# Optimization experiments

Measured on AMD Instinct MI355X. Metric: run time of the kernel, lower is better.

## Reference

```python
import jax, jax.numpy as jnp
import numpy as np

B, N, H, W, C_OUT = 4, 480000, 1024, 1024, 64
PR = (0.0, -39.68, -3.0, 69.12, 39.68, 1.0)  # point cloud range [x0,y0,z0,x1,y1,z1]
BN_EPS = 1e-5


def setup_inputs():
    key = jax.random.key(0)
    ks = iter(jax.random.split(key, 48))
    bidx = jax.random.randint(next(ks), (N,), 0, B).astype(jnp.float32)
    px = jax.random.uniform(next(ks), (N,), minval=PR[0], maxval=PR[3])
    py = jax.random.uniform(next(ks), (N,), minval=PR[1], maxval=PR[4])
    pz = jax.random.uniform(next(ks), (N,), minval=PR[2], maxval=PR[5])
    pi = jax.random.uniform(next(ks), (N,))
    points = jnp.stack([bidx, px, py, pz, pi], axis=1)  # [N,5]

    def w(shape):
        return jax.random.normal(next(ks), shape, jnp.float32) * 0.1

    def bnp(c):
        return (1.0 + 0.1 * jax.random.normal(next(ks), (c,), jnp.float32),
                0.1 * jax.random.normal(next(ks), (c,), jnp.float32),
                0.1 * jax.random.normal(next(ks), (c,), jnp.float32),
                jax.random.uniform(next(ks), (c,), minval=0.5, maxval=1.5))

    g0, be0, m0, v0 = bnp(8)
    g1, be1, m1, v1 = bnp(16)
    g2, be2, m2, v2 = bnp(32)
    g3, be3, m3, v3 = bnp(C_OUT)
    return {
        'points': points, 'batch_size': B,
        'w0': w((8, 2, 3, 3)), 'b0': w((8,)),
        'g0': g0, 'be0': be0, 'm0': m0, 'v0': v0,
        'w1': w((16, 1, 3, 3)), 'b1': w((16,)),  # groups=8 conv: 16 out, 8 in groups
        'g1': g1, 'be1': be1, 'm1': m1, 'v1': v1,
        'wdw': w((16, 1, 3, 3)), 'bdw': w((16,)),
        'wpw': w((32, 16, 1, 1)), 'bpw': w((32,)),
        'g2': g2, 'be2': be2, 'm2': m2, 'v2': v2,
        'w3': w((C_OUT, 32, 3, 3)), 'b3': w((C_OUT,)),
        'g3': g3, 'be3': be3, 'm3': m3, 'v3': v3,
    }


def conv2d(x, wt, b, groups=1, pad=1):
    out = jax.lax.conv_general_dilated(
        x, wt, (1, 1), [(pad, pad), (pad, pad)],
        feature_group_count=groups,
        dimension_numbers=('NCHW', 'OIHW', 'NCHW'))
    return out + b[None, :, None, None]


def bn(x, g, be, m, v):
    s = g * jax.lax.rsqrt(v + BN_EPS)
    return x * s[None, :, None, None] + (be - m * s)[None, :, None, None]


def maxpool2(x):
    return jax.lax.reduce_window(x, -jnp.inf, jax.lax.max,
                                 (1, 1, 2, 2), (1, 1, 2, 2), 'VALID')


def channel_shuffle(x, groups):
    b, c, h, w = x.shape
    return x.reshape(b, groups, c // groups, h, w).transpose(0, 2, 1, 3, 4).reshape(b, c, h, w)


def rasterize(points, batch_size):
    # points: [N,5] = (batch_idx, x, y, z, intensity)
    x_scale = W / (PR[3] - PR[0])
    y_scale = H / (PR[4] - PR[1])
    # PR[0]==0 -> no x shift (matches the source's branch)
    xp = (points[:, 1] * x_scale).astype(jnp.int32)  # trunc toward zero like torch .to(int)
    yp = ((points[:, 2] + (PR[4] - PR[1]) / 2) * y_scale).astype(jnp.int32)
    valid = (xp >= 0) & (xp < W) & (yp >= 0) & (yp < H)
    bi = jnp.where(valid, points[:, 0].astype(jnp.int32), batch_size)  # invalid -> OOB, dropped
    xi = jnp.where(valid, xp, W)
    yi = jnp.where(valid, yp, H)
    bev_z = jnp.full((batch_size, H, W), -10.0, jnp.float32)
    bev_z = bev_z.at[bi, yi, xi].max(points[:, 3], mode='drop')
    bev_i = jnp.zeros((batch_size, H, W), jnp.float32)
    bev_i = bev_i.at[bi, yi, xi].max(points[:, 4], mode='drop')
    return jnp.stack([bev_z, bev_i], axis=1)  # [B,2,H,W]


def reference(points, batch_size, w0, b0, g0, be0, m0, v0, w1, b1, g1, be1, m1, v1,
              wdw, bdw, wpw, bpw, g2, be2, m2, v2, w3, b3, g3, be3, m3, v3):
    x = rasterize(points, batch_size)
    x = jax.nn.relu(bn(conv2d(x, w0, b0), g0, be0, m0, v0))          # x_conv1
    x = maxpool2(x)
    x = jax.nn.relu(bn(conv2d(x, w1, b1, groups=8), g1, be1, m1, v1))  # x_conv2
    x = maxpool2(x)
    x = conv2d(x, wdw, bdw, groups=16)      # depthwise
    x = channel_shuffle(x, 16)              # identity when groups==channels, kept for faithfulness
    x = conv2d(x, wpw, bpw, pad=0)          # pointwise 16->32
    x = jax.nn.relu(bn(x, g2, be2, m2, v2))
    x = jax.nn.relu(bn(conv2d(x, w3, b3), g3, be3, m3, v3))          # x_conv3
    x = maxpool2(x)                         # x_conv4 == spatial_features
    return x
```

## Files before the change

### kernel.cpp

```cpp
#include <hip/hip_runtime.h>
#include <cstddef>

#define H_IN 1024
#define W_IN 1024
#define BN_EPS 1e-5f

typedef float f32x4 __attribute__((ext_vector_type(4)));
typedef _Float16 f16x8 __attribute__((ext_vector_type(8)));

__device__ __forceinline__ unsigned encF(float f) {
    unsigned u = __float_as_uint(f);
    return (u & 0x80000000u) ? ~u : (u | 0x80000000u);
}
__device__ __forceinline__ float decF(unsigned e, float untouched) {
    if (e == 0u) return untouched;
    unsigned bits = (e & 0x80000000u) ? (e ^ 0x80000000u) : ~e;
    return __uint_as_float(bits);
}

__global__ void k_rasterize(const float* __restrict__ pts, unsigned* __restrict__ bev, int n) {
    int i = blockIdx.x * blockDim.x + threadIdx.x;
    if (i >= n) return;
    float fb  = pts[(size_t)i*5+0];
    float px  = pts[(size_t)i*5+1];
    float py  = pts[(size_t)i*5+2];
    float pz  = pts[(size_t)i*5+3];
    float pit = pts[(size_t)i*5+4];
    const float XS = (float)(1024.0/69.12);
    const float YS = (float)(1024.0/79.36);
    int xp = (int)(px * XS);
    int yp = (int)((py + 39.68f) * YS);
    if (xp < 0 || xp >= W_IN || yp < 0 || yp >= H_IN) return;
    int b = (int)fb;
    size_t off = (((size_t)b * H_IN + yp) * W_IN + xp) * 2;
    atomicMax(bev + off,     encF(pz));
    atomicMax(bev + off + 1, encF(pit));
}

__global__ __launch_bounds__(256, 4) void k_conv1(
                        const unsigned* __restrict__ bev, const float* __restrict__ w0,
                        const float* __restrict__ b0, const float* __restrict__ g0,
                        const float* __restrict__ be0, const float* __restrict__ m0,
                        const float* __restrict__ v0, _Float16* __restrict__ out) {
    __shared__ float wS[144];
    __shared__ float sS[8], tS[8];
    int t = threadIdx.x;
    if (t < 144) wS[t] = w0[t];
    if (t < 8) {
        float s = g0[t] / sqrtf(v0[t] + BN_EPS);
        sS[t] = s;
        tS[t] = (b0[t] - m0[t]) * s + be0[t];
    }
    __syncthreads();
    int idx = blockIdx.x * 256 + t;
    int x = idx & 511, y = (idx >> 9) & 511, b = idx >> 18;
    const unsigned* base = bev + (size_t)b * H_IN * W_IN * 2;
    float in[2][4][4];
    #pragma unroll
    for (int r = 0; r < 4; r++) {
        int iy = 2*y - 1 + r;
        #pragma unroll
        for (int cc = 0; cc < 4; cc++) {
            int ix = 2*x - 1 + cc;
            if (iy >= 0 && iy < H_IN && ix >= 0 && ix < W_IN) {
                const unsigned* p2 = base + ((size_t)iy*W_IN + ix)*2;
                in[0][r][cc] = decF(p2[0], -10.0f);
                in[1][r][cc] = decF(p2[1], 0.0f);
            } else {
                in[0][r][cc] = 0.0f;
                in[1][r][cc] = 0.0f;
            }
        }
    }
    f16x8 ov;
    #pragma unroll
    for (int oc = 0; oc < 8; oc++) {
        float mx = 0.0f;
        #pragma unroll
        for (int py = 0; py < 2; py++)
            #pragma unroll
            for (int px = 0; px < 2; px++) {
                float acc = 0.0f;
                #pragma unroll
                for (int c = 0; c < 2; c++)
                    #pragma unroll
                    for (int kh = 0; kh < 3; kh++)
                        #pragma unroll
                        for (int kw = 0; kw < 3; kw++)
                            acc += in[c][py+kh][px+kw] * wS[((oc*2+c)*3+kh)*3+kw];
                acc = fmaxf(acc * sS[oc] + tS[oc], 0.0f);
                mx = fmaxf(mx, acc);
            }
        ov[oc] = (_Float16)mx;
    }
    *(f16x8*)(out + ((size_t)((b*512 + y)*512 + x)) * 8) = ov;
}

__global__ __launch_bounds__(256, 4) void k_conv2(
                        const _Float16* __restrict__ x1, const float* __restrict__ w1,
                        const float* __restrict__ b1, const float* __restrict__ g1,
                        const float* __restrict__ be1, const float* __restrict__ m1,
                        const float* __restrict__ v1, float* __restrict__ out) {
    __shared__ float wS[144];
    __shared__ float sS[16], tS[16];
    int t = threadIdx.x;
    if (t < 144) wS[t] = w1[t];
    if (t < 16) {
        float s = g1[t] / sqrtf(v1[t] + BN_EPS);
        sS[t] = s;
        tS[t] = (b1[t] - m1[t]) * s + be1[t];
    }
    __syncthreads();
    int idx = blockIdx.x * 256 + t;
    int x = idx & 255, y = (idx >> 8) & 255, b = idx >> 16;
    const _Float16* base = x1 + (size_t)b * 512 * 512 * 8;

    f16x8 p[4][4];
    #pragma unroll
    for (int r = 0; r < 4; r++) {
        int iy = 2*y - 1 + r;
        #pragma unroll
        for (int c = 0; c < 4; c++) {
            int ix = 2*x - 1 + c;
            if (iy >= 0 && iy < 512 && ix >= 0 && ix < 512) {
                p[r][c] = *(const f16x8*)(base + ((size_t)iy*512 + ix)*8);
            } else {
                f16x8 z = {0,0,0,0,0,0,0,0};
                p[r][c] = z;
            }
        }
    }

    float* ob = out + (size_t)b * 16 * 256 * 256 + (size_t)y*256 + x;
    #pragma unroll
    for (int g = 0; g < 8; g++) {
        #pragma unroll
        for (int sub = 0; sub < 2; sub++) {
            int oc = g*2 + sub;
            float mx = 0.0f;
            #pragma unroll
            for (int qy = 0; qy < 2; qy++)
                #pragma unroll
                for (int qx = 0; qx < 2; qx++) {
                    float acc = 0.0f;
                    #pragma unroll
                    for (int kh = 0; kh < 3; kh++)
                        #pragma unroll
                        for (int kw = 0; kw < 3; kw++)
                            acc += (float)p[qy+kh][qx+kw][g] * wS[(oc*3+kh)*3+kw];
                    acc = fmaxf(acc * sS[oc] + tS[oc], 0.0f);
                    mx = fmaxf(mx, acc);
                }
            ob[(size_t)oc*65536] = mx;
        }
    }
}

__global__ __launch_bounds__(256, 4) void k_dwpw(
                       const float* __restrict__ x2, const float* __restrict__ wdw,
                       const float* __restrict__ bdw, const float* __restrict__ wpw,
                       const float* __restrict__ bpw, const float* __restrict__ g2,
                       const float* __restrict__ be2, const float* __restrict__ m2,
                       const float* __restrict__ v2, _Float16* __restrict__ out) {
    __shared__ float patch[16*10*36];
    __shared__ float wdwS[144];
    __shared__ float bdwS[16];
    __shared__ float wpwS[512];
    __shared__ float sS[32], tS[32];
    int t = threadIdx.x;
    if (t < 144) wdwS[t] = wdw[t];
    if (t < 16) bdwS[t] = bdw[t];
    for (int i = t; i < 512; i += 256) wpwS[i] = wpw[i];
    if (t < 32) {
        float s = g2[t] / sqrtf(v2[t] + BN_EPS);
        sS[t] = s;
        tS[t] = (bpw[t] - m2[t]) * s + be2[t];
    }

    int bi = blockIdx.x;
    int tx = bi & 7, ty = (bi >> 3) & 31, b = bi >> 8;
    int x0 = tx * 32, y0 = ty * 8;
    const float* base = x2 + (size_t)b * 16 * 256 * 256;

    for (int i = t; i < 16*10*34; i += 256) {
        int ic = i / 340;
        int rem = i - ic * 340;
        int r = rem / 34, c = rem - r * 34;
        int gy = y0 - 1 + r, gx = x0 - 1 + c;
        patch[(ic*10 + r)*36 + c] =
            (gy >= 0 && gy < 256 && gx >= 0 && gx < 256)
                ? base[(size_t)ic*65536 + (size_t)gy*256 + gx] : 0.0f;
    }
    __syncthreads();

    int px = t & 31, pyy = t >> 5;
    int x = x0 + px, y = y0 + pyy;

    float dv[16];
    #pragma unroll
    for (int ic = 0; ic < 16; ic++) {
        float d = bdwS[ic];
        #pragma unroll
        for (int r = 0; r < 3; r++)
            #pragma unroll
            for (int c = 0; c < 3; c++)
                d += patch[(ic*10 + pyy + r)*36 + px + c] * wdwS[ic*9 + r*3 + c];
        dv[ic] = d;
    }

    _Float16* ob = out + ((size_t)((b*256 + y)*256 + x)) * 32;
    #pragma unroll
    for (int q = 0; q < 4; q++) {
        f16x8 ov;
        #pragma unroll
        for (int j = 0; j < 8; j++) {
            int oc = q*8 + j;
            float a = 0.0f;
            #pragma unroll
            for (int ic = 0; ic < 16; ic++)
                a += dv[ic] * wpwS[oc*16+ic];
            ov[j] = (_Float16)fmaxf(a*sS[oc] + tS[oc], 0.0f);
        }
        *(f16x8*)(ob + q*8) = ov;
    }
}

__global__ void k_wprep(const float* __restrict__ w3, const float* __restrict__ b3,
                        const float* __restrict__ g3, const float* __restrict__ be3,
                        const float* __restrict__ m3, const float* __restrict__ v3,
                        _Float16* __restrict__ wh, float* __restrict__ tv) {
    __shared__ float sSh[64];
    int t = threadIdx.x;
    if (t < 64) {
        float s = g3[t] / sqrtf(v3[t] + BN_EPS);
        sSh[t] = s;
        if (blockIdx.x == 0) tv[t] = (b3[t] - m3[t]) * s + be3[t];
    }
    __syncthreads();
    int khw = blockIdx.x;
    for (int i = t; i < 2048; i += 256) {
        int oc = i >> 5;
        wh[khw*2048 + i] = (_Float16)(w3[(size_t)i*9 + khw] * sSh[oc]);
    }
}

__global__ __launch_bounds__(256, 2) void k_conv3m(const _Float16* __restrict__ xh,
                                                   const _Float16* __restrict__ wh,
                                                   const float* __restrict__ tv,
                                                   float* __restrict__ out) {
    __shared__ _Float16 As[10*66*40];
    int t = threadIdx.x;
    int lane = t & 63, w = t >> 6;
    int l15 = lane & 15, l4 = lane >> 4;
    int bi = blockIdx.x;
    int xt = bi & 3, yg = (bi >> 2) & 31, b = bi >> 7;
    int x0 = xt * 64;
    int y0 = yg * 8;

    f16x8 Bf[9][4];
    #pragma unroll
    for (int khw = 0; khw < 9; khw++)
        #pragma unroll
        for (int g = 0; g < 4; g++)
            Bf[khw][g] = *(const f16x8*)(wh + ((khw*64 + g*16 + l15)*32 + 8*l4));

    float tvv[4];
    #pragma unroll
    for (int g = 0; g < 4; g++) tvv[g] = tv[g*16 + l15];

    for (int s = t; s < 660; s += 256) {
        int row = s / 66, px = s - row*66;
        int gy = y0 - 1 + row, gx = x0 - 1 + px;
        float4* dst = (float4*)&As[(row*66 + px)*40];
        if (gy >= 0 && gy < 256 && gx >= 0 && gx < 256) {
            const float4* src = (const float4*)(xh + ((size_t)((b*256 + gy)*256 + gx)) * 32);
            #pragma unroll
            for (int j = 0; j < 4; j++) dst[j] = src[j];
        } else {
            float4 z = make_float4(0.f, 0.f, 0.f, 0.f);
            #pragma unroll
            for (int j = 0; j < 4; j++) dst[j] = z;
        }
    }
    __syncthreads();

    for (int ti = 0; ti < 4; ti++) {
        int ypool = yg*4 + ti;
        f32x4 acc[2][4];
        #pragma unroll
        for (int f = 0; f < 2; f++)
            #pragma unroll
            for (int g = 0; g < 4; g++)
                acc[f][g] = (f32x4){0.f, 0.f, 0.f, 0.f};

        #pragma unroll
        for (int kh = 0; kh < 3; kh++)
            #pragma unroll
            for (int kw = 0; kw < 3; kw++) {
                f16x8 Af[2];
                #pragma unroll
                for (int f = 0; f < 2; f++) {
                    int row = 2*ti + f + kh;
                    int px = w*16 + l15 + kw;
                    Af[f] = *(const f16x8*)&As[(row*66 + px)*40 + 8*l4];
                }
                #pragma unroll
                for (int f = 0; f < 2; f++)
                    #pragma unroll
                    for (int g = 0; g < 4; g++)
                        acc[f][g] = __builtin_amdgcn_mfma_f32_16x16x32_f16(
                            Af[f], Bf[kh*3+kw][g], acc[f][g], 0, 0, 0);
            }

        #pragma unroll
        for (int g = 0; g < 4; g++) {
            int oc = g*16 + l15;
            #pragma unroll
            for (int q = 0; q < 2; q++) {
                float v0 = fmaxf(fmaxf(acc[0][g][2*q]   + tvv[g], 0.f),
                                 fmaxf(acc[0][g][2*q+1] + tvv[g], 0.f));
                float v1 = fmaxf(fmaxf(acc[1][g][2*q]   + tvv[g], 0.f),
                                 fmaxf(acc[1][g][2*q+1] + tvv[g], 0.f));
                int px = x0/2 + w*8 + 2*l4 + q;
                out[(((size_t)b*64 + oc)*128 + ypool)*128 + px] = fmaxf(v0, v1);
            }
        }
    }
}

extern "C" void kernel_launch(void* const* d_in, const int* in_sizes, int n_in,
                              void* d_out, int out_size, void* d_ws, size_t ws_size,
                              hipStream_t stream) {
    const float* points = (const float*)d_in[0];
    int n = in_sizes[0] / 5;
    const float* w0  = (const float*)d_in[2];
    const float* b0  = (const float*)d_in[3];
    const float* g0  = (const float*)d_in[4];
    const float* be0 = (const float*)d_in[5];
    const float* m0  = (const float*)d_in[6];
    const float* v0  = (const float*)d_in[7];
    const float* w1  = (const float*)d_in[8];
    const float* b1  = (const float*)d_in[9];
    const float* g1  = (const float*)d_in[10];
    const float* be1 = (const float*)d_in[11];
    const float* m1  = (const float*)d_in[12];
    const float* v1  = (const float*)d_in[13];
    const float* wdw = (const float*)d_in[14];
    const float* bdw = (const float*)d_in[15];
    const float* wpw = (const float*)d_in[16];
    const float* bpw = (const float*)d_in[17];
    const float* g2  = (const float*)d_in[18];
    const float* be2 = (const float*)d_in[19];
    const float* m2  = (const float*)d_in[20];
    const float* v2  = (const float*)d_in[21];
    const float* w3  = (const float*)d_in[22];
    const float* b3  = (const float*)d_in[23];
    const float* g3  = (const float*)d_in[24];
    const float* be3 = (const float*)d_in[25];
    const float* m3  = (const float*)d_in[26];
    const float* v3  = (const float*)d_in[27];

    float* ws  = (float*)d_ws;
    unsigned* bev = (unsigned*)ws;
    _Float16* x1h = (_Float16*)(ws + 8388608);
    float* x2  = ws;
    _Float16* x3h = (_Float16*)(ws + 8388608);
    _Float16* wh  = (_Float16*)(ws + 16777216);
    float* tv  = ws + 16786432;
    float* outp = (float*)d_out;

    k_wprep<<<9, 256, 0, stream>>>(w3, b3, g3, be3, m3, v3, wh, tv);
    hipMemsetAsync(bev, 0, (size_t)4 * H_IN * W_IN * 2 * sizeof(unsigned), stream);
    k_rasterize<<<(n + 255)/256, 256, 0, stream>>>(points, bev, n);
    k_conv1<<<4096, 256, 0, stream>>>(bev, w0, b0, g0, be0, m0, v0, x1h);
    k_conv2<<<1024, 256, 0, stream>>>(x1h, w1, b1, g1, be1, m1, v1, x2);
    k_dwpw<<<1024, 256, 0, stream>>>(x2, wdw, bdw, wpw, bpw, g2, be2, m2, v2, x3h);
    k_conv3m<<<512, 256, 0, stream>>>(x3h, wh, tv, outp);
}
```

Measured before the change: 142.2 us.

## Rewrite grouped conv2 as MFMA over LDS tile, fuse memset with weight prep

The grouped 3x3 conv2 with maxpool now loads a 10x66 input tile into shared memory and computes it with 16x16x32 f16 MFMA instructions, using per-kw zero-padded weight fragments, instead of per-thread scalar FMAs over a 4x4 register patch. The BEV memset and the conv3 weight prep are merged into one launch, and rasterization uses a grid-stride loop with a quarter as many blocks. The aim is less ALU work in conv2 and fewer launches, at the cost of wasted MFMA lanes and new index mapping that could be wrong.

```diff
diff --git a/kernel.cpp b/kernel.cpp
--- a/kernel.cpp
+++ b/kernel.cpp
@@ -18,23 +18,54 @@
     return __uint_as_float(bits);
 }
 
+__global__ void k_prep(uint4* __restrict__ bevq,
+                       const float* __restrict__ w3, const float* __restrict__ b3,
+                       const float* __restrict__ g3, const float* __restrict__ be3,
+                       const float* __restrict__ m3, const float* __restrict__ v3,
+                       _Float16* __restrict__ wh, float* __restrict__ tv) {
+    int bid = blockIdx.x;
+    int t = threadIdx.x;
+    if (bid < 2048) {
+        int i = bid * 256 + t;
+        uint4 z = {0u, 0u, 0u, 0u};
+        #pragma unroll
+        for (int j = 0; j < 4; j++)
+            bevq[(size_t)j*524288 + i] = z;
+        return;
+    }
+    __shared__ float sSh[64];
+    if (t < 64) {
+        float s = g3[t] / sqrtf(v3[t] + BN_EPS);
+        sSh[t] = s;
+        if (bid == 2048) tv[t] = (b3[t] - m3[t]) * s + be3[t];
+    }
+    __syncthreads();
+    int khw = bid - 2048;
+    for (int i = t; i < 2048; i += 256) {
+        int oc = i >> 5;
+        wh[khw*2048 + i] = (_Float16)(w3[(size_t)i*9 + khw] * sSh[oc]);
+    }
+}
+
 __global__ void k_rasterize(const float* __restrict__ pts, unsigned* __restrict__ bev, int n) {
-    int i = blockIdx.x * blockDim.x + threadIdx.x;
-    if (i >= n) return;
-    float fb  = pts[(size_t)i*5+0];
-    float px  = pts[(size_t)i*5+1];
-    float py  = pts[(size_t)i*5+2];
-    float pz  = pts[(size_t)i*5+3];
-    float pit = pts[(size_t)i*5+4];
+    int i0 = blockIdx.x * blockDim.x + threadIdx.x;
+    int stride = gridDim.x * blockDim.x;
     const float XS = (float)(1024.0/69.12);
     const float YS = (float)(1024.0/79.36);
-    int xp = (int)(px * XS);
-    int yp = (int)((py + 39.68f) * YS);
-    if (xp < 0 || xp >= W_IN || yp < 0 || yp >= H_IN) return;
-    int b = (int)fb;
-    size_t off = (((size_t)b * H_IN + yp) * W_IN + xp) * 2;
-    atomicMax(bev + off,     encF(pz));
-    atomicMax(bev + off + 1, encF(pit));
+    for (int i = i0; i < n; i += stride) {
+        float fb  = pts[(size_t)i*5+0];
+        float px  = pts[(size_t)i*5+1];
+        float py  = pts[(size_t)i*5+2];
+        float pz  = pts[(size_t)i*5+3];
+        float pit = pts[(size_t)i*5+4];
+        int xp = (int)(px * XS);
+        int yp = (int)((py + 39.68f) * YS);
+        if (xp < 0 || xp >= W_IN || yp < 0 || yp >= H_IN) continue;
+        int b = (int)fb;
+        size_t off = (((size_t)b * H_IN + yp) * W_IN + xp) * 2;
+        atomicMax(bev + off,     encF(pz));
+        atomicMax(bev + off + 1, encF(pit));
+    }
 }
 
 __global__ __launch_bounds__(256, 4) void k_conv1(
@@ -96,13 +127,13 @@
     *(f16x8*)(out + ((size_t)((b*512 + y)*512 + x)) * 8) = ov;
 }
 
-__global__ __launch_bounds__(256, 4) void k_conv2(
+__global__ __launch_bounds__(256, 4) void k_conv2m(
                         const _Float16* __restrict__ x1, const float* __restrict__ w1,
                         const float* __restrict__ b1, const float* __restrict__ g1,
                         const float* __restrict__ be1, const float* __restrict__ m1,
                         const float* __restrict__ v1, float* __restrict__ out) {
-    __shared__ float wS[144];
-    __shared__ float sS[16], tS[16];
+    __shared__ _Float16 As[10][66][8];
+    __shared__ float wS[144], sS[16], tS[16];
     int t = threadIdx.x;
     if (t < 144) wS[t] = w1[t];
     if (t < 16) {
@@ -110,48 +141,57 @@
         sS[t] = s;
         tS[t] = (b1[t] - m1[t]) * s + be1[t];
     }
-    __syncthreads();
-    int idx = blockIdx.x * 256 + t;
-    int x = idx & 255, y = (idx >> 8) & 255, b = idx >> 16;
+    int lane = t & 63, w = t >> 6;
+    int l15 = lane & 15, l4 = lane >> 4;
+    int bi = blockIdx.x;
+    int xt = bi & 7, yg = (bi >> 3) & 63, b = bi >> 9;
+    int x0 = xt * 64;
+    int y0 = yg * 8;
+    __syncthreads();
+
+    f16x8 Bf[3];
+    #pragma unroll
+    for (int kh = 0; kh < 3; kh++) {
+        f16x8 z = {0,0,0,0,0,0,0,0};
+        if (l4 < 3) z[l15 >> 1] = (_Float16)(wS[l15*9 + kh*3 + l4] * sS[l15]);
+        Bf[kh] = z;
+    }
+    float tvv = tS[l15];
+
     const _Float16* base = x1 + (size_t)b * 512 * 512 * 8;
-
-    f16x8 p[4][4];
-    #pragma unroll
-    for (int r = 0; r < 4; r++) {
-        int iy = 2*y - 1 + r;
-        #pragma unroll
-        for (int c = 0; c < 4; c++) {
-            int ix = 2*x - 1 + c;
-            if (iy >= 0 && iy < 512 && ix >= 0 && ix < 512) {
-                p[r][c] = *(const f16x8*)(base + ((size_t)iy*512 + ix)*8);
-            } else {
-                f16x8 z = {0,0,0,0,0,0,0,0};
-                p[r][c] = z;
+    for (int s = t; s < 660; s += 256) {
+        int row = s / 66, px = s - row * 66;
+        int gy = y0 - 1 + row, gx = x0 - 1 + px;
+        f16x8 v = {0,0,0,0,0,0,0,0};
+        if (gy >= 0 && gy < 512 && gx >= 0 && gx < 512)
+            v = *(const f16x8*)(base + ((size_t)gy*512 + gx)*8);
+        *(f16x8*)&As[row][px][0] = v;
+    }
+    __syncthreads();
+
+    for (int ti = 0; ti < 4; ti++) {
+        f32x4 acc[2];
+        acc[0] = (f32x4){0,0,0,0};
+        acc[1] = (f32x4){0,0,0,0};
+        #pragma unroll
+        for (int kh = 0; kh < 3; kh++)
+            #pragma unroll
+            for (int f = 0; f < 2; f++) {
+                f16x8 Af = {0,0,0,0,0,0,0,0};
+                if (l4 < 3)
+                    Af = *(const f16x8*)&As[2*ti + f + kh][w*16 + l15 + l4][0];
+                acc[f] = __builtin_amdgcn_mfma_f32_16x16x32_f16(Af, Bf[kh], acc[f], 0, 0, 0);
             }
-        }
-    }
-
-    float* ob = out + (size_t)b * 16 * 256 * 256 + (size_t)y*256 + x;
-    #pragma unroll
-    for (int g = 0; g < 8; g++) {
-        #pragma unroll
-        for (int sub = 0; sub < 2; sub++) {
-            int oc = g*2 + sub;
-            float mx = 0.0f;
-            #pragma unroll
-            for (int qy = 0; qy < 2; qy++)
-                #pragma unroll
-                for (int qx = 0; qx < 2; qx++) {
-                    float acc = 0.0f;
-                    #pragma unroll
-                    for (int kh = 0; kh < 3; kh++)
-                        #pragma unroll
-                        for (int kw = 0; kw < 3; kw++)
-                            acc += (float)p[qy+kh][qx+kw][g] * wS[(oc*3+kh)*3+kw];
-                    acc = fmaxf(acc * sS[oc] + tS[oc], 0.0f);
-                    mx = fmaxf(mx, acc);
-                }
-            ob[(size_t)oc*65536] = mx;
+        int yp = yg*4 + ti;
+        float* ob = out + (size_t)b*16*65536 + (size_t)l15*65536 + (size_t)yp*256;
+        #pragma unroll
+        for (int q = 0; q < 2; q++) {
+            float v0 = fmaxf(fmaxf(acc[0][2*q]   + tvv, 0.f),
+                             fmaxf(acc[0][2*q+1] + tvv, 0.f));
+            float v1_ = fmaxf(fmaxf(acc[1][2*q]   + tvv, 0.f),
+                              fmaxf(acc[1][2*q+1] + tvv, 0.f));
+            int xp = xt*32 + w*8 + 2*l4 + q;
+            ob[xp] = fmaxf(v0, v1_);
         }
     }
 }
@@ -222,25 +262,6 @@
             ov[j] = (_Float16)fmaxf(a*sS[oc] + tS[oc], 0.0f);
         }
         *(f16x8*)(ob + q*8) = ov;
-    }
-}
-
-__global__ void k_wprep(const float* __restrict__ w3, const float* __restrict__ b3,
-                        const float* __restrict__ g3, const float* __restrict__ be3,
-                        const float* __restrict__ m3, const float* __restrict__ v3,
-                        _Float16* __restrict__ wh, float* __restrict__ tv) {
-    __shared__ float sSh[64];
-    int t = threadIdx.x;
-    if (t < 64) {
-        float s = g3[t] / sqrtf(v3[t] + BN_EPS);
-        sSh[t] = s;
-        if (blockIdx.x == 0) tv[t] = (b3[t] - m3[t]) * s + be3[t];
-    }
-    __syncthreads();
-    int khw = blockIdx.x;
-    for (int i = t; i < 2048; i += 256) {
-        int oc = i >> 5;
-        wh[khw*2048 + i] = (_Float16)(w3[(size_t)i*9 + khw] * sSh[oc]);
     }
 }
 
@@ -369,11 +390,11 @@
     float* tv  = ws + 16786432;
     float* outp = (float*)d_out;
 
-    k_wprep<<<9, 256, 0, stream>>>(w3, b3, g3, be3, m3, v3, wh, tv);
-    hipMemsetAsync(bev, 0, (size_t)4 * H_IN * W_IN * 2 * sizeof(unsigned), stream);
-    k_rasterize<<<(n + 255)/256, 256, 0, stream>>>(points, bev, n);
+    k_prep<<<2057, 256, 0, stream>>>((uint4*)bev, w3, b3, g3, be3, m3, v3, wh, tv);
+    int rblocks = (n/4 + 255) / 256;
+    k_rasterize<<<rblocks, 256, 0, stream>>>(points, bev, n);
     k_conv1<<<4096, 256, 0, stream>>>(bev, w0, b0, g0, be0, m0, v0, x1h);
-    k_conv2<<<1024, 256, 0, stream>>>(x1h, w1, b1, g1, be1, m1, v1, x2);
+    k_conv2m<<<2048, 256, 0, stream>>>(x1h, w1, b1, g1, be1, m1, v1, x2);
     k_dwpw<<<1024, 256, 0, stream>>>(x2, wdw, bdw, wpw, bpw, g2, be2, m2, v2, x3h);
     k_conv3m<<<512, 256, 0, stream>>>(x3h, wh, tv, outp);
 }
```

Result: faster. 133.2 us (-6.3%).
